# Kernel optimization log

Measured on AMD Instinct MI355X. Metric: run time of the kernel, lower is better.

Reference implementation:

```python
import jax, jax.numpy as jnp
import numpy as np

NQ, NK, H, DH = 1024, 512, 8, 64


def setup_inputs() -> dict:
    key = jax.random.key(0)
    ks = jax.random.split(key, 8)
    b, n, d, g = 4, 4096, 1024, 4
    di = H * DH  # 512
    s = lambda fan: 1.0 / np.sqrt(fan)
    return {
        "x": jax.random.normal(ks[0], (b, n, d), jnp.float32),
        "w_qr": jax.random.normal(ks[1], (g, d), jnp.float32) * s(d),
        "w_kvr": jax.random.normal(ks[2], (g, d), jnp.float32) * s(d),
        "w_q": jax.random.normal(ks[3], (g, di, d), jnp.float32) * s(d),
        "w_kv": jax.random.normal(ks[4], (g, 2 * di, d), jnp.float32) * s(d),
        "w_out": jax.random.normal(ks[5], (g, d, di), jnp.float32) * s(di),
        "null_kv": jax.random.normal(ks[6], (2, g, H, 1, DH), jnp.float32),
        "null_token": jax.random.normal(ks[7], (1, 1, d), jnp.float32),
    }


def reference(x, w_qr, w_kvr, w_q, w_kv, w_out, null_kv, null_token):
    b, n, d = x.shape
    g = w_qr.shape[0]
    bidx = jnp.arange(b)[:, None, None]
    # --- routing: per-expert token scores, top-k select (router reference) ---
    q_logits = jnp.einsum("bnd,gd->bgn", x, w_qr)
    q_top, q_idx = jax.lax.top_k(q_logits, NQ)            # [b,g,NQ]
    q_scores = jax.nn.sigmoid(q_top)[..., None]           # [b,g,NQ,1]
    queries = x[bidx, q_idx]                              # [b,g,NQ,d]
    kv_logits = jnp.einsum("bnd,gd->bgn", x, w_kvr)
    kv_top, kv_idx = jax.lax.top_k(kv_logits, NK)
    kv_scores = jax.nn.sigmoid(kv_top)[:, :, None, :, None]  # [b,g,1,NK,1]
    key_values = x[bidx, kv_idx]                          # [b,g,NK,d]
    # --- grouped attention (1x1 grouped convs == per-group matmuls) ---
    q = jnp.einsum("bgnd,ged->bgne", queries, w_q)
    kv = jnp.einsum("bgnd,ged->bgne", key_values, w_kv)
    k, v = jnp.split(kv, 2, axis=-1)
    heads = lambda t: t.reshape(b, g, -1, H, DH).transpose(0, 1, 3, 2, 4)  # b g h n dh
    q, k, v = heads(q), heads(k), heads(v)
    v = v * kv_scores                                     # values_scale
    nk = jnp.broadcast_to(null_kv[0][None], (b, g, H, 1, DH))
    nv = jnp.broadcast_to(null_kv[1][None], (b, g, H, 1, DH))
    k = jnp.concatenate([nk, k], axis=-2)
    v = jnp.concatenate([nv, v], axis=-2)
    attn = jax.nn.softmax(jnp.einsum("bghid,bghjd->bghij", q, k) * DH ** -0.5, axis=-1)
    o = jnp.einsum("bghij,bghjd->bghid", attn, v)
    o = o.transpose(0, 1, 3, 2, 4).reshape(b, g, NQ, H * DH)
    o = jnp.einsum("bgne,gde->bgnd", o, w_out)
    o = o * q_scores
    # --- scatter-add back with count normalization ---
    flat_idx = q_idx.reshape(b, g * NQ)
    flat_o = o.reshape(b, g * NQ, d)
    b2 = jnp.arange(b)[:, None]
    summed = jnp.zeros_like(x).at[b2, flat_idx].add(flat_o)
    counts = jnp.zeros((b, n), x.dtype).at[b2, flat_idx].add(1.0)[..., None]
    meaned = summed / jnp.clip(counts, 1e-5)
    return jnp.where(counts > 0, meaned, null_token)
```

## Files before the change

### kernel.cpp

```cpp
#include <hip/hip_runtime.h>
#include <math.h>

#define NB 4
#define SEQ 4096
#define DM 1024
#define NG 4
#define DI 512
#define NQS 1024
#define NKS 512
#define NHD 8
#define DHD 64
#define VTS 520

typedef unsigned int u32;
typedef unsigned short u16;
typedef __bf16 bf16x8 __attribute__((ext_vector_type(8)));
typedef float f32x4 __attribute__((ext_vector_type(4)));

__device__ __forceinline__ float bf2f(u16 u) { return __uint_as_float(((u32)u) << 16); }
__device__ __forceinline__ u16 f2bf(float f) {
  u32 u = __float_as_uint(f);
  u32 r = (u + 0x7FFFu + ((u >> 16) & 1u)) >> 16;
  return (u16)r;
}
__device__ __forceinline__ u16 f2bfh(float f) {
  union { __bf16 b; u16 u; } cv;
  cv.b = (__bf16)f;
  return cv.u;
}

__global__ __launch_bounds__(256) void router_kernel(
    const float* __restrict__ x, const float* __restrict__ wqr,
    const float* __restrict__ wkvr, float* __restrict__ qlog,
    float* __restrict__ kvlog, u16* __restrict__ xbf) {
  int tid = threadIdx.x;
  int base = blockIdx.x * 8 + (tid >> 6) * 2;
  int lane = tid & 63;
  int b = base >> 12, tok = base & 4095;
  const float4* xr0 = (const float4*)(x + ((size_t)(b * SEQ + tok)) * DM);
  const float4* xr1 = xr0 + 256;
  float4 xv0[4], xv1[4];
#pragma unroll
  for (int i = 0; i < 4; i++) {
    xv0[i] = xr0[i * 64 + lane];
    xv1[i] = xr1[i * 64 + lane];
  }
  ushort4* xrow0 = (ushort4*)(xbf + ((size_t)(b * SEQ + tok)) * DM);
  ushort4* xrow1 = xrow0 + 256;
#pragma unroll
  for (int i = 0; i < 4; i++) {
    ushort4 o0, o1;
    o0.x = f2bf(xv0[i].x); o0.y = f2bf(xv0[i].y);
    o0.z = f2bf(xv0[i].z); o0.w = f2bf(xv0[i].w);
    o1.x = f2bf(xv1[i].x); o1.y = f2bf(xv1[i].y);
    o1.z = f2bf(xv1[i].z); o1.w = f2bf(xv1[i].w);
    xrow0[i * 64 + lane] = o0;
    xrow1[i * 64 + lane] = o1;
  }
  float a0[8], a1[8];
#pragma unroll
  for (int r = 0; r < 8; r++) {
    const float4* wr =
        (const float4*)(r < 4 ? wqr + (r << 10) : wkvr + ((r - 4) << 10));
    float s0 = 0.f, s1 = 0.f;
#pragma unroll
    for (int i = 0; i < 4; i++) {
      float4 w4 = wr[i * 64 + lane];
      s0 += xv0[i].x * w4.x + xv0[i].y * w4.y + xv0[i].z * w4.z + xv0[i].w * w4.w;
      s1 += xv1[i].x * w4.x + xv1[i].y * w4.y + xv1[i].z * w4.z + xv1[i].w * w4.w;
    }
    a0[r] = s0; a1[r] = s1;
  }
#pragma unroll
  for (int r = 0; r < 8; r++) {
#pragma unroll
    for (int off = 32; off >= 1; off >>= 1) {
      a0[r] += __shfl_xor(a0[r], off);
      a1[r] += __shfl_xor(a1[r], off);
    }
    if (lane == 0) {
      if (r < 4) {
        qlog[((b << 2) | r) * SEQ + tok] = a0[r];
        qlog[((b << 2) | r) * SEQ + tok + 1] = a1[r];
      } else {
        kvlog[((b << 2) | (r - 4)) * SEQ + tok] = a0[r];
        kvlog[((b << 2) | (r - 4)) * SEQ + tok + 1] = a1[r];
      }
    }
  }
}

__global__ __launch_bounds__(256) void topk_kernel(
    const float* __restrict__ qlog, const float* __restrict__ kvlog,
    int* __restrict__ qidx, float* __restrict__ qscore,
    int* __restrict__ kvidx, float* __restrict__ kvscore,
    int* __restrict__ qpos, const float* __restrict__ wq,
    const float* __restrict__ wkv, const float* __restrict__ wout,
    u16* __restrict__ wqbf, u16* __restrict__ wkvbf, u16* __restrict__ woutbf) {
  int tid = threadIdx.x;
  if (blockIdx.x >= 32) {
    int cid = blockIdx.x - 32;
#pragma unroll
    for (int j = 0; j < 4; j++) {
      int idx = cid * 1024 + j * 256 + tid;
      const float* src; u16* dst; int off;
      if (idx < 524288)        { src = wq;   dst = wqbf;   off = idx; }
      else if (idx < 1572864)  { src = wkv;  dst = wkvbf;  off = idx - 524288; }
      else                     { src = wout; dst = woutbf; off = idx - 1572864; }
      float4 v = ((const float4*)src)[off];
      ushort4 o;
      o.x = f2bf(v.x); o.y = f2bf(v.y); o.z = f2bf(v.z); o.w = f2bf(v.w);
      ((ushort4*)dst)[off] = o;
    }
    return;
  }
  __shared__ u32 keys[4096];
  __shared__ int eqlist[2048];
  __shared__ int scnt[4];
  __shared__ int s_gt, s_eq;
  int which = blockIdx.x >> 4;
  int bg = blockIdx.x & 15;
  int K = (which == 0) ? NQS : NKS;
  const float* L = ((which == 0) ? qlog : kvlog) + bg * 4096;
  int* out_idx = ((which == 0) ? qidx : kvidx) + bg * K;
  float* out_score = ((which == 0) ? qscore : kvscore) + bg * K;
  int* qposb = qpos + bg * 4096;
  for (int e = tid; e < 4096; e += 256) {
    u32 u = __float_as_uint(L[e]);
    keys[e] = (u >> 31) ? ~u : (u | 0x80000000u);
  }
  if (which == 0)
    for (int e = tid; e < 4096; e += 256) qposb[e] = -1;
  if (tid == 0) { s_gt = 0; s_eq = 0; }
  __syncthreads();
  u32 prefix = 0;
  int remaining = K;
  for (int bit = 31; bit >= 12; --bit) {
    u32 want = prefix | (1u << bit);
    u32 mask = ~((1u << bit) - 1u);
    int c = 0;
    for (int e = tid; e < 4096; e += 256) c += ((keys[e] & mask) == want) ? 1 : 0;
#pragma unroll
    for (int off = 32; off >= 1; off >>= 1) c += __shfl_xor(c, off);
    if ((tid & 63) == 0) scnt[tid >> 6] = c;
    __syncthreads();
    int total = scnt[0] + scnt[1] + scnt[2] + scnt[3];
    if (total >= remaining) prefix = want;
    else remaining -= total;
    __syncthreads();
  }
  u32 T = prefix;
  for (int e = tid; e < 4096; e += 256) {
    u32 k = keys[e];
    u32 k20 = k & 0xFFFFF000u;
    if (k20 > T) {
      int pos = atomicAdd(&s_gt, 1);
      out_idx[pos] = e;
      u32 uo = (k >> 31) ? (k & 0x7FFFFFFFu) : ~k;
      float v = __uint_as_float(uo);
      out_score[pos] = 1.0f / (1.0f + __expf(-v));
      if (which == 0) qposb[e] = pos;
    } else if (k20 == T) {
      int p = atomicAdd(&s_eq, 1);
      if (p < 2048) eqlist[p] = e;
    }
  }
  __syncthreads();
  int gt = s_gt;
  int eq = min(s_eq, 2048);
  int need = K - gt;
  for (int i = tid; i < eq; i += 256) {
    int my = eqlist[i];
    u32 myk = keys[my];
    int rank = 0;
    for (int j = 0; j < eq; j++) {
      u32 kj = keys[eqlist[j]];
      rank += (kj > myk || (kj == myk && eqlist[j] < my)) ? 1 : 0;
    }
    if (rank < need) {
      int pos = gt + rank;
      out_idx[pos] = my;
      u32 uo = (myk >> 31) ? (myk & 0x7FFFFFFFu) : ~myk;
      float v = __uint_as_float(uo);
      out_score[pos] = 1.0f / (1.0f + __expf(-v));
      if (which == 0) qposb[my] = pos;
    }
  }
}

struct Ptr4 { const u16* p[4]; };

__device__ __forceinline__ void mfma_core(Ptr4 A, Ptr4 B, u16* Asm, u16* Bsm,
                                          int ktiles, int tid, f32x4 (&acc)[4][4]) {
  int w = tid >> 6, lane = tid & 63;
  int col = lane & 15, quad = lane >> 4;
  int wr = w >> 1, wc = w & 1;
  for (int kt = 0; kt < ktiles; kt++) {
#pragma unroll
    for (int r = 0; r < 4; r++) {
      char* ldsA = (char*)Asm + (r * 256 + w * 64) * 16;
      __builtin_amdgcn_global_load_lds(
          (const __attribute__((address_space(1))) void*)(A.p[r] + kt * 64),
          (__attribute__((address_space(3))) void*)ldsA, 16, 0, 0);
    }
#pragma unroll
    for (int r = 0; r < 4; r++) {
      char* ldsB = (char*)Bsm + (r * 256 + w * 64) * 16;
      __builtin_amdgcn_global_load_lds(
          (const __attribute__((address_space(1))) void*)(B.p[r] + kt * 64),
          (__attribute__((address_space(3))) void*)ldsB, 16, 0, 0);
    }
    __syncthreads();
#pragma unroll
    for (int k04 = 0; k04 < 8; k04 += 4) {
      bf16x8 af[4], bfr[4];
#pragma unroll
      for (int t = 0; t < 4; t++) {
        int rowa = wr * 64 + t * 16 + col;
        int sp = (quad + k04) ^ (col & 7);
        af[t] = *(const bf16x8*)((const char*)Asm + (rowa * 8 + sp) * 16);
        int rowb = wc * 64 + t * 16 + col;
        bfr[t] = *(const bf16x8*)((const char*)Bsm + (rowb * 8 + sp) * 16);
      }
#pragma unroll
      for (int t = 0; t < 4; t++)
#pragma unroll
        for (int u = 0; u < 4; u++)
          acc[t][u] = __builtin_amdgcn_mfma_f32_16x16x32_bf16(af[t], bfr[u], acc[t][u], 0, 0, 0);
    }
    __syncthreads();
  }
}

__global__ __launch_bounds__(256) void gemm_qkvproj(
    const u16* __restrict__ xbf, const int* __restrict__ qidx,
    const int* __restrict__ kvidx, const u16* __restrict__ wqbf,
    const u16* __restrict__ wkvbf, const float* __restrict__ kvscore,
    u16* __restrict__ qbuf, u16* __restrict__ kbuf, u16* __restrict__ vtbuf) {
  __shared__ __align__(16) u16 Asm[8192], Bsm[8192];
  __shared__ int ridx[128];
  int tid = threadIdx.x;
  int id = blockIdx.x;
  bool is_q = (id & 1) == 0;
  int sid = id >> 1;
  int bg = sid >> 5, r5 = sid & 31;
  int b = bg >> 2, g = bg & 3;
  int w = tid >> 6, lane = tid & 63;
  int col = lane & 15, quad = lane >> 4;
  int wr = w >> 1, wc = w & 1;

  if (is_q) {
    int col0 = (r5 & 3) * 128, row0 = (r5 >> 2) * 128;
    if (tid < 128) ridx[tid] = qidx[bg * NQS + row0 + tid];
    __syncthreads();
    Ptr4 A, B;
#pragma unroll
    for (int r = 0; r < 4; r++) {
      int G = r * 256 + tid;
      int row = G >> 3;
      int seg = (G & 7) ^ (row & 7);
      A.p[r] = xbf + ((size_t)b * SEQ + ridx[row]) * DM + seg * 8;
      B.p[r] = wqbf + ((size_t)g * DI + col0 + row) * DM + seg * 8;
    }
    f32x4 acc[4][4] = {};
    mfma_core(A, B, Asm, Bsm, DM / 64, tid, acc);
#pragma unroll
    for (int t = 0; t < 4; t++)
#pragma unroll
      for (int u = 0; u < 4; u++)
#pragma unroll
        for (int r = 0; r < 4; r++) {
          int rowg = row0 + wr * 64 + t * 16 + quad * 4 + r;
          int colg = col0 + wc * 64 + u * 16 + col;
          qbuf[((size_t)bg * NQS + rowg) * DI + colg] = f2bf(acc[t][u][r] * 0.125f);
        }
  } else {
    int col0 = (r5 & 7) * 128, row0 = (r5 >> 3) * 128;
    if (tid < 128) ridx[tid] = kvidx[bg * NKS + row0 + tid];
    __syncthreads();
    Ptr4 A, B;
#pragma unroll
    for (int r = 0; r < 4; r++) {
      int G = r * 256 + tid;
      int row = G >> 3;
      int seg = (G & 7) ^ (row & 7);
      A.p[r] = xbf + ((size_t)b * SEQ + ridx[row]) * DM + seg * 8;
      B.p[r] = wkvbf + ((size_t)g * (2 * DI) + col0 + row) * DM + seg * 8;
    }
    f32x4 acc[4][4] = {};
    mfma_core(A, B, Asm, Bsm, DM / 64, tid, acc);
    if (col0 < DI) {
#pragma unroll
      for (int t = 0; t < 4; t++)
#pragma unroll
        for (int u = 0; u < 4; u++)
#pragma unroll
          for (int r = 0; r < 4; r++) {
            int rowg = row0 + wr * 64 + t * 16 + quad * 4 + r;
            int colg = col0 + wc * 64 + u * 16 + col;
            kbuf[((size_t)bg * NKS + rowg) * DI + colg] = f2bf(acc[t][u][r]);
          }
    } else {
#pragma unroll
      for (int t = 0; t < 4; t++) {
        int base = row0 + wr * 64 + t * 16 + quad * 4;
        float sc0 = kvscore[bg * NKS + base + 0];
        float sc1 = kvscore[bg * NKS + base + 1];
        float sc2 = kvscore[bg * NKS + base + 2];
        float sc3 = kvscore[bg * NKS + base + 3];
#pragma unroll
        for (int u = 0; u < 4; u++) {
          int vc = col0 - DI + wc * 64 + u * 16 + col;
          int h = vc >> 6, d = vc & 63;
          u32 lo = (u32)f2bf(acc[t][u][0] * sc0) | ((u32)f2bf(acc[t][u][1] * sc1) << 16);
          u32 hi = (u32)f2bf(acc[t][u][2] * sc2) | ((u32)f2bf(acc[t][u][3] * sc3) << 16);
          *(uint2*)&vtbuf[(((size_t)bg * NHD + h) * DHD + d) * VTS + base] =
              make_uint2(lo, hi);
        }
      }
    }
  }
}

__global__ __launch_bounds__(256) void gemm_outproj(
    const u16* __restrict__ obuf, const u16* __restrict__ woutbf,
    const float* __restrict__ qscore, u16* __restrict__ oproj_lo,
    u16* __restrict__ oproj_hi) {
  int bg = blockIdx.z, g = bg & 3;
  int row0 = blockIdx.y * 128, col0 = blockIdx.x * 128;
  __shared__ __align__(16) u16 Asm[8192], Bsm[8192];
  int tid = threadIdx.x;
  Ptr4 A, B;
#pragma unroll
  for (int r = 0; r < 4; r++) {
    int G = r * 256 + tid;
    int row = G >> 3;
    int seg = (G & 7) ^ (row & 7);
    A.p[r] = obuf + ((size_t)bg * NQS + row0 + row) * DI + seg * 8;
    B.p[r] = woutbf + ((size_t)g * DM + col0 + row) * DI + seg * 8;
  }
  f32x4 acc[4][4] = {};
  mfma_core(A, B, Asm, Bsm, DI / 64, tid, acc);
  int w = tid >> 6, lane = tid & 63;
  int col = lane & 15, quad = lane >> 4;
  int wr = w >> 1, wc = w & 1;
  u16* obase = (bg < 8 ? oproj_lo : oproj_hi) + (size_t)(bg & 7) * NQS * DM;
#pragma unroll
  for (int t = 0; t < 4; t++)
#pragma unroll
    for (int r = 0; r < 4; r++) {
      int rowg = row0 + wr * 64 + t * 16 + quad * 4 + r;
      float sc = qscore[bg * NQS + rowg];
      u16* orow = obase + (size_t)rowg * DM;
#pragma unroll
      for (int u = 0; u < 4; u++) {
        int colg = col0 + wc * 64 + u * 16 + col;
        orow[colg] = f2bfh(acc[t][u][r] * sc);
      }
    }
}

__global__ __launch_bounds__(256) void finalize_gather(
    const u16* __restrict__ oproj_lo, const u16* __restrict__ oproj_hi,
    const int* __restrict__ qpos, const float* __restrict__ null_token,
    float* __restrict__ dout) {
  int blk = blockIdx.x;
  int b = blk >> 12;
  int tok = blk & 4095;
  int tid = threadIdx.x;
  const u16* obase = (b < 2) ? oproj_lo : oproj_hi;
  int zoff = (b & 1) * 4;
  float4 acc = {0.f, 0.f, 0.f, 0.f};
  int cnt = 0;
#pragma unroll
  for (int g = 0; g < 4; g++) {
    int pos = qpos[(((b << 2) | g)) * 4096 + tok];
    if (pos >= 0) {
      const uint2* row =
          (const uint2*)(obase + ((size_t)(zoff + g) * NQS + pos) * DM);
      uint2 v = row[tid];
      acc.x += bf2f((u16)(v.x & 0xFFFF));
      acc.y += bf2f((u16)(v.x >> 16));
      acc.z += bf2f((u16)(v.y & 0xFFFF));
      acc.w += bf2f((u16)(v.y >> 16));
      cnt++;
    }
  }
  float4* dst = (float4*)(dout + ((size_t)b * SEQ + tok) * DM) + tid;
  if (cnt > 0) {
    float inv = 1.0f / cnt;
    acc.x *= inv; acc.y *= inv; acc.z *= inv; acc.w *= inv;
    *dst = acc;
  } else {
    *dst = ((const float4*)null_token)[tid];
  }
}

__global__ __launch_bounds__(256, 4) void attn_mfma(
    const u16* __restrict__ qbuf, const u16* __restrict__ kbuf,
    const u16* __restrict__ vtbuf, const float* __restrict__ null_kv,
    u16* __restrict__ obuf) {
  int id = blockIdx.x;
  int qt = id >> 7;
  int h = id & 7;
  int bg = (id >> 3) & 15;
  int g = bg & 3;
  int tid = threadIdx.x;
  int w = tid >> 6, lane = tid & 63;
  int col = lane & 15, quad = lane >> 4;

  __shared__ __align__(16) u16 Ks[64][72];
  __shared__ __align__(16) u16 Vts[64][72];
  __shared__ __align__(16) u16 Ps[4][32][72];

  int q0 = qt * 128 + w * 32;
  const u16* qp0 = qbuf + ((size_t)bg * NQS + q0 + col) * DI + h * DHD + quad * 8;
  bf16x8 qa[2][2];
  qa[0][0] = *(const bf16x8*)qp0;
  qa[0][1] = *(const bf16x8*)(qp0 + 32);
  qa[1][0] = *(const bf16x8*)(qp0 + 16 * DI);
  qa[1][1] = *(const bf16x8*)(qp0 + 16 * DI + 32);

  const float* kn = null_kv + ((size_t)(0 * NG + g) * NHD + h) * DHD;
  const float* vn = null_kv + ((size_t)(1 * NG + g) * NHD + h) * DHD;
  float m_run[2], l_lane[2];
  f32x4 oacc[2][4];
#pragma unroll
  for (int s = 0; s < 2; s++) {
    float sn = 0.f;
#pragma unroll
    for (int i = 0; i < 8; i++) {
      sn += (float)qa[s][0][i] * kn[quad * 8 + i];
      sn += (float)qa[s][1][i] * kn[32 + quad * 8 + i];
    }
    sn += __shfl_xor(sn, 16);
    sn += __shfl_xor(sn, 32);
    m_run[s] = sn;
    l_lane[s] = (quad == 0) ? 1.f : 0.f;
  }
#pragma unroll
  for (int t = 0; t < 4; t++) {
    float v = vn[t * 16 + col];
    f32x4 tmp = {v, v, v, v};
    oacc[0][t] = tmp;
    oacc[1][t] = tmp;
  }

  int sr = tid >> 2, ss = tid & 3;
  const u16* kptr = kbuf + ((size_t)bg * NKS + sr) * DI + h * DHD + ss * 16;
  const u16* vptr = vtbuf + (((size_t)bg * NHD + h) * DHD + sr) * VTS + ss * 16;
  uint4* kdst = (uint4*)&Ks[sr][ss * 16];
  uint4* vdst = (uint4*)&Vts[sr][ss * 16];
  uint4 ck0, ck1, cv0, cv1;
  { const uint4* p = (const uint4*)kptr; ck0 = p[0]; ck1 = p[1]; }
  { const uint4* p = (const uint4*)vptr; cv0 = p[0]; cv1 = p[1]; }

  for (int c = 0; c < 8; ++c) {
    kdst[0] = ck0; kdst[1] = ck1;
    vdst[0] = cv0; vdst[1] = cv1;
    if (c < 7) {
      const uint4* p = (const uint4*)(kptr + (size_t)(c + 1) * 64 * DI);
      ck0 = p[0]; ck1 = p[1];
      const uint4* q4 = (const uint4*)(vptr + (c + 1) * 64);
      cv0 = q4[0]; cv1 = q4[1];
    }
    __syncthreads();

    f32x4 sv[2][4];
#pragma unroll
    for (int t = 0; t < 4; t++) {
      bf16x8 kb0 = *(const bf16x8*)&Ks[t * 16 + col][quad * 8];
      bf16x8 kb1 = *(const bf16x8*)&Ks[t * 16 + col][quad * 8 + 32];
      f32x4 z = {0.f, 0.f, 0.f, 0.f};
      f32x4 s0 = __builtin_amdgcn_mfma_f32_16x16x32_bf16(kb0, qa[0][0], z, 0, 0, 0);
      sv[0][t] = __builtin_amdgcn_mfma_f32_16x16x32_bf16(kb1, qa[0][1], s0, 0, 0, 0);
      f32x4 s1 = __builtin_amdgcn_mfma_f32_16x16x32_bf16(kb0, qa[1][0], z, 0, 0, 0);
      sv[1][t] = __builtin_amdgcn_mfma_f32_16x16x32_bf16(kb1, qa[1][1], s1, 0, 0, 0);
    }

#pragma unroll
    for (int s = 0; s < 2; s++) {
      float pm = sv[s][0][0];
#pragma unroll
      for (int t = 0; t < 4; t++)
#pragma unroll
        for (int r = 0; r < 4; r++) pm = fmaxf(pm, sv[s][t][r]);
      pm = fmaxf(pm, __shfl_xor(pm, 16));
      pm = fmaxf(pm, __shfl_xor(pm, 32));
      if (!__all(pm <= m_run[s] + 8.0f)) {
        float mnew = fmaxf(m_run[s], pm);
        float alpha = __expf(m_run[s] - mnew);
        m_run[s] = mnew;
        l_lane[s] *= alpha;
#pragma unroll
        for (int r = 0; r < 4; r++) {
          float a_o = __shfl(alpha, quad * 4 + r);
#pragma unroll
          for (int t = 0; t < 4; t++) oacc[s][t][r] *= a_o;
        }
      }
      float rs = 0.f;
#pragma unroll
      for (int t = 0; t < 4; t++) {
        float p0 = __expf(sv[s][t][0] - m_run[s]);
        float p1 = __expf(sv[s][t][1] - m_run[s]);
        float p2 = __expf(sv[s][t][2] - m_run[s]);
        float p3 = __expf(sv[s][t][3] - m_run[s]);
        rs += (p0 + p1) + (p2 + p3);
        u32 lo = (u32)f2bfh(p0) | ((u32)f2bfh(p1) << 16);
        u32 hi = (u32)f2bfh(p2) | ((u32)f2bfh(p3) << 16);
        *(uint2*)&Ps[w][s * 16 + col][t * 16 + quad * 4] = make_uint2(lo, hi);
      }
      l_lane[s] += rs;
    }

#pragma unroll
    for (int s2 = 0; s2 < 2; s2++) {
      bf16x8 pa0 = *(const bf16x8*)&Ps[w][col][s2 * 32 + quad * 8];
      bf16x8 pa1 = *(const bf16x8*)&Ps[w][16 + col][s2 * 32 + quad * 8];
#pragma unroll
      for (int t = 0; t < 4; t++) {
        bf16x8 vb = *(const bf16x8*)&Vts[t * 16 + col][s2 * 32 + quad * 8];
        oacc[0][t] = __builtin_amdgcn_mfma_f32_16x16x32_bf16(pa0, vb, oacc[0][t], 0, 0, 0);
        oacc[1][t] = __builtin_amdgcn_mfma_f32_16x16x32_bf16(pa1, vb, oacc[1][t], 0, 0, 0);
      }
    }
    __syncthreads();
  }

#pragma unroll
  for (int s = 0; s < 2; s++) {
    float l = l_lane[s];
    l += __shfl_xor(l, 16);
    l += __shfl_xor(l, 32);
    float inv = 1.0f / l;
#pragma unroll
    for (int r = 0; r < 4; r++) {
      float ir = __shfl(inv, quad * 4 + r);
#pragma unroll
      for (int t = 0; t < 4; t++) {
        obuf[((size_t)bg * NQS + q0 + s * 16 + quad * 4 + r) * DI + h * DHD +
             t * 16 + col] = f2bfh(oacc[s][t][r] * ir);
      }
    }
  }
}

extern "C" void kernel_launch(void* const* d_in, const int* in_sizes, int n_in,
                              void* d_out, int out_size, void* d_ws, size_t ws_size,
                              hipStream_t stream) {
  const float* x = (const float*)d_in[0];
  const float* wqr = (const float*)d_in[1];
  const float* wkvr = (const float*)d_in[2];
  const float* wq = (const float*)d_in[3];
  const float* wkv = (const float*)d_in[4];
  const float* wout = (const float*)d_in[5];
  const float* nullkv = (const float*)d_in[6];
  const float* nulltok = (const float*)d_in[7];
  float* out = (float*)d_out;
  char* ws = (char*)d_ws;
  float* qlog = (float*)(ws + 0);
  float* kvlog = (float*)(ws + 262144);
  int* qidx = (int*)(ws + 524288);
  int* kvidx = (int*)(ws + 589824);
  float* qscore = (float*)(ws + 622592);
  float* kvscore = (float*)(ws + 688128);
  u16* qbuf = (u16*)(ws + 786432);
  u16* kbuf = (u16*)(ws + 17563648);
  u16* vtbuf = (u16*)(ws + 25952256);
  u16* obuf = (u16*)(ws + 34476032);
  u16* xbf = (u16*)(ws + 51253248);
  u16* wqbf = (u16*)(ws + 84807680);
  u16* wkvbf = (u16*)(ws + 89001984);
  u16* woutbf = (u16*)(ws + 97390592);
  int* qpos = (int*)(ws + 0);
  u16* oproj_lo = (u16*)(ws + 786432);
  u16* oproj_hi = (u16*)(ws + 51253248);

  router_kernel<<<2048, 256, 0, stream>>>(x, wqr, wkvr, qlog, kvlog, xbf);
  topk_kernel<<<2080, 256, 0, stream>>>(qlog, kvlog, qidx, qscore, kvidx,
                                        kvscore, qpos, wq, wkv, wout, wqbf,
                                        wkvbf, woutbf);
  gemm_qkvproj<<<1024, 256, 0, stream>>>(xbf, qidx, kvidx, wqbf, wkvbf, kvscore,
                                         qbuf, kbuf, vtbuf);
  attn_mfma<<<1024, 256, 0, stream>>>(qbuf, kbuf, vtbuf, nullkv, obuf);
  gemm_outproj<<<dim3(8, 8, 16), 256, 0, stream>>>(obuf, woutbf, qscore,
                                                   oproj_lo, oproj_hi);
  finalize_gather<<<16384, 256, 0, stream>>>(oproj_lo, oproj_hi, qpos, nulltok,
                                             out);
}
```

Baseline: 301.1 us.

## Double-buffer GEMM LDS tiles and use 2-bit radix steps in top-k select

The shared MFMA GEMM core now ping-pongs between two LDS buffers, issuing the global-to-LDS load for the next k-tile before computing on the current one, so load latency can overlap with MFMA work. This doubles LDS per block, which may lower occupancy. Separately, the top-k radix threshold search resolves two bits per pass using three bucket counts, halving the number of passes and barriers over the 4096 keys.

```diff
diff --git a/kernel.cpp b/kernel.cpp
--- a/kernel.cpp
+++ b/kernel.cpp
@@ -116,7 +116,7 @@
   }
   __shared__ u32 keys[4096];
   __shared__ int eqlist[2048];
-  __shared__ int scnt[4];
+  __shared__ int scnt[12];
   __shared__ int s_gt, s_eq;
   int which = blockIdx.x >> 4;
   int bg = blockIdx.x & 15;
@@ -135,18 +135,34 @@
   __syncthreads();
   u32 prefix = 0;
   int remaining = K;
-  for (int bit = 31; bit >= 12; --bit) {
-    u32 want = prefix | (1u << bit);
-    u32 mask = ~((1u << bit) - 1u);
-    int c = 0;
-    for (int e = tid; e < 4096; e += 256) c += ((keys[e] & mask) == want) ? 1 : 0;
-#pragma unroll
-    for (int off = 32; off >= 1; off >>= 1) c += __shfl_xor(c, off);
-    if ((tid & 63) == 0) scnt[tid >> 6] = c;
+  for (int bit = 30; bit >= 12; bit -= 2) {
+    u32 maskhi = (bit >= 30) ? 0u : (0xFFFFFFFFu << (bit + 2));
+    int c3 = 0, c2 = 0, c1 = 0;
+    for (int e = tid; e < 4096; e += 256) {
+      u32 k = keys[e];
+      if ((k & maskhi) == prefix) {
+        u32 bkt = (k >> bit) & 3u;
+        c3 += (bkt == 3u); c2 += (bkt == 2u); c1 += (bkt == 1u);
+      }
+    }
+#pragma unroll
+    for (int off = 32; off >= 1; off >>= 1) {
+      c3 += __shfl_xor(c3, off);
+      c2 += __shfl_xor(c2, off);
+      c1 += __shfl_xor(c1, off);
+    }
+    if ((tid & 63) == 0) {
+      int wv = tid >> 6;
+      scnt[wv * 3 + 0] = c3; scnt[wv * 3 + 1] = c2; scnt[wv * 3 + 2] = c1;
+    }
     __syncthreads();
-    int total = scnt[0] + scnt[1] + scnt[2] + scnt[3];
-    if (total >= remaining) prefix = want;
-    else remaining -= total;
+    int n3 = scnt[0] + scnt[3] + scnt[6] + scnt[9];
+    int n2 = scnt[1] + scnt[4] + scnt[7] + scnt[10];
+    int n1 = scnt[2] + scnt[5] + scnt[8] + scnt[11];
+    if (n3 >= remaining) prefix |= 3u << bit;
+    else if (n3 + n2 >= remaining) { prefix |= 2u << bit; remaining -= n3; }
+    else if (n3 + n2 + n1 >= remaining) { prefix |= 1u << bit; remaining -= n3 + n2; }
+    else remaining -= (n3 + n2 + n1);
     __syncthreads();
   }
   u32 T = prefix;
@@ -190,27 +206,37 @@
 
 struct Ptr4 { const u16* p[4]; };
 
-__device__ __forceinline__ void mfma_core(Ptr4 A, Ptr4 B, u16* Asm, u16* Bsm,
-                                          int ktiles, int tid, f32x4 (&acc)[4][4]) {
+__device__ __forceinline__ void stage_tile(const Ptr4& A, const Ptr4& B,
+                                           u16* Asmb, u16* Bsmb, int kt, int w) {
+#pragma unroll
+  for (int r = 0; r < 4; r++) {
+    char* ldsA = (char*)Asmb + (r * 256 + w * 64) * 16;
+    __builtin_amdgcn_global_load_lds(
+        (const __attribute__((address_space(1))) void*)(A.p[r] + kt * 64),
+        (__attribute__((address_space(3))) void*)ldsA, 16, 0, 0);
+  }
+#pragma unroll
+  for (int r = 0; r < 4; r++) {
+    char* ldsB = (char*)Bsmb + (r * 256 + w * 64) * 16;
+    __builtin_amdgcn_global_load_lds(
+        (const __attribute__((address_space(1))) void*)(B.p[r] + kt * 64),
+        (__attribute__((address_space(3))) void*)ldsB, 16, 0, 0);
+  }
+}
+
+__device__ __forceinline__ void mfma_core(Ptr4 A, Ptr4 B, u16* Asm0, u16* Bsm0,
+                                          u16* Asm1, u16* Bsm1, int ktiles,
+                                          int tid, f32x4 (&acc)[4][4]) {
   int w = tid >> 6, lane = tid & 63;
   int col = lane & 15, quad = lane >> 4;
   int wr = w >> 1, wc = w & 1;
+  stage_tile(A, B, Asm0, Bsm0, 0, w);
+  __syncthreads();
   for (int kt = 0; kt < ktiles; kt++) {
-#pragma unroll
-    for (int r = 0; r < 4; r++) {
-      char* ldsA = (char*)Asm + (r * 256 + w * 64) * 16;
-      __builtin_amdgcn_global_load_lds(
-          (const __attribute__((address_space(1))) void*)(A.p[r] + kt * 64),
-          (__attribute__((address_space(3))) void*)ldsA, 16, 0, 0);
-    }
-#pragma unroll
-    for (int r = 0; r < 4; r++) {
-      char* ldsB = (char*)Bsm + (r * 256 + w * 64) * 16;
-      __builtin_amdgcn_global_load_lds(
-          (const __attribute__((address_space(1))) void*)(B.p[r] + kt * 64),
-          (__attribute__((address_space(3))) void*)ldsB, 16, 0, 0);
-    }
-    __syncthreads();
+    const u16* Ac = (kt & 1) ? Asm1 : Asm0;
+    const u16* Bc = (kt & 1) ? Bsm1 : Bsm0;
+    if (kt + 1 < ktiles)
+      stage_tile(A, B, (kt & 1) ? Asm0 : Asm1, (kt & 1) ? Bsm0 : Bsm1, kt + 1, w);
 #pragma unroll
     for (int k04 = 0; k04 < 8; k04 += 4) {
       bf16x8 af[4], bfr[4];
@@ -218,9 +244,9 @@
       for (int t = 0; t < 4; t++) {
         int rowa = wr * 64 + t * 16 + col;
         int sp = (quad + k04) ^ (col & 7);
-        af[t] = *(const bf16x8*)((const char*)Asm + (rowa * 8 + sp) * 16);
+        af[t] = *(const bf16x8*)((const char*)Ac + (rowa * 8 + sp) * 16);
         int rowb = wc * 64 + t * 16 + col;
-        bfr[t] = *(const bf16x8*)((const char*)Bsm + (rowb * 8 + sp) * 16);
+        bfr[t] = *(const bf16x8*)((const char*)Bc + (rowb * 8 + sp) * 16);
       }
 #pragma unroll
       for (int t = 0; t < 4; t++)
@@ -237,7 +263,7 @@
     const int* __restrict__ kvidx, const u16* __restrict__ wqbf,
     const u16* __restrict__ wkvbf, const float* __restrict__ kvscore,
     u16* __restrict__ qbuf, u16* __restrict__ kbuf, u16* __restrict__ vtbuf) {
-  __shared__ __align__(16) u16 Asm[8192], Bsm[8192];
+  __shared__ __align__(16) u16 Asm[2][8192], Bsm[2][8192];
   __shared__ int ridx[128];
   int tid = threadIdx.x;
   int id = blockIdx.x;
@@ -263,7 +289,7 @@
       B.p[r] = wqbf + ((size_t)g * DI + col0 + row) * DM + seg * 8;
     }
     f32x4 acc[4][4] = {};
-    mfma_core(A, B, Asm, Bsm, DM / 64, tid, acc);
+    mfma_core(A, B, Asm[0], Bsm[0], Asm[1], Bsm[1], DM / 64, tid, acc);
 #pragma unroll
     for (int t = 0; t < 4; t++)
 #pragma unroll
@@ -288,7 +314,7 @@
       B.p[r] = wkvbf + ((size_t)g * (2 * DI) + col0 + row) * DM + seg * 8;
     }
     f32x4 acc[4][4] = {};
-    mfma_core(A, B, Asm, Bsm, DM / 64, tid, acc);
+    mfma_core(A, B, Asm[0], Bsm[0], Asm[1], Bsm[1], DM / 64, tid, acc);
     if (col0 < DI) {
 #pragma unroll
       for (int t = 0; t < 4; t++)
@@ -328,7 +354,7 @@
     u16* __restrict__ oproj_hi) {
   int bg = blockIdx.z, g = bg & 3;
   int row0 = blockIdx.y * 128, col0 = blockIdx.x * 128;
-  __shared__ __align__(16) u16 Asm[8192], Bsm[8192];
+  __shared__ __align__(16) u16 Asm[2][8192], Bsm[2][8192];
   int tid = threadIdx.x;
   Ptr4 A, B;
 #pragma unroll
@@ -340,7 +366,7 @@
     B.p[r] = woutbf + ((size_t)g * DM + col0 + row) * DI + seg * 8;
   }
   f32x4 acc[4][4] = {};
-  mfma_core(A, B, Asm, Bsm, DI / 64, tid, acc);
+  mfma_core(A, B, Asm[0], Bsm[0], Asm[1], Bsm[1], DI / 64, tid, acc);
   int w = tid >> 6, lane = tid & 63;
   int col = lane & 15, quad = lane >> 4;
   int wr = w >> 1, wc = w & 1;
```

After: 294.8 us. 2.1% less time.
